# Kernel tuning notes

Measured on AMD Instinct MI355X. Metric: run time of the kernel, lower is better.

The kernel has to match this reference:

```python
import jax, jax.numpy as jnp
import numpy as np

N, C, H, W = 64, 64, 8, 8        # batch, img_net_out_dim, feature-map spatial dims
E = 256                           # ques_rnn_hidden_dim
G = 256                           # rn_g_dim
F_DIM = 256                       # rn_f_dim
NUM_CLASSES = 2
D = C + 2                         # per-object feature dim (channels + 2 loc coords)
G_IN = 2 * D + E                  # 388


def setup_inputs() -> dict:
    key = jax.random.key(0)
    ks = jax.random.split(key, 10)

    def w(k, shape):
        fan_in = shape[0]
        return jax.random.normal(k, shape, dtype=jnp.float32) / np.sqrt(fan_in).astype(np.float32)

    return {
        "img": jax.random.normal(ks[0], (N, C, H, W), dtype=jnp.float32),
        "ques": jax.random.normal(ks[1], (N, E), dtype=jnp.float32),
        "g_w1": w(ks[2], (G_IN, G)), "g_b1": jnp.zeros((G,), jnp.float32),
        "g_w2": w(ks[3], (G, G)),    "g_b2": jnp.zeros((G,), jnp.float32),
        "g_w3": w(ks[4], (G, G)),    "g_b3": jnp.zeros((G,), jnp.float32),
        "g_w4": w(ks[5], (G, G)),    "g_b4": jnp.zeros((G,), jnp.float32),
        "f_w1": w(ks[6], (G, F_DIM)),       "f_b1": jnp.zeros((F_DIM,), jnp.float32),
        "f_w2": w(ks[7], (F_DIM, F_DIM)),   "f_b2": jnp.zeros((F_DIM,), jnp.float32),
        "f_w3": w(ks[8], (F_DIM, NUM_CLASSES)), "f_b3": jnp.zeros((NUM_CLASSES,), jnp.float32),
    }


def _img_to_pairs(img, ques):
    # img: (N, C, H, W); ques: (N, E) -> pairs: (N, O*O, 2*(C+2)+E)
    n, c, h, w = img.shape
    o = h * w
    cells = img.reshape(n, c, o)
    idx = jnp.arange(o)
    loc = jnp.stack([idx // w, idx % w], axis=0).astype(img.dtype)      # (2, O)
    cells = jnp.concatenate([cells, jnp.broadcast_to(loc, (n, 2, o))], axis=1)  # (N, D, O)
    cells = cells.transpose(0, 2, 1)                                    # (N, O, D)
    d = cells.shape[-1]
    one = jnp.broadcast_to(cells[:, :, None, :], (n, o, o, d))          # object i
    two = jnp.broadcast_to(cells[:, None, :, :], (n, o, o, d))          # object j
    three = jnp.broadcast_to(ques[:, None, None, :], (n, o, o, ques.shape[-1]))
    pairs = jnp.concatenate([one, two, three], axis=-1)                 # (N, O, O, G_IN)
    return pairs.reshape(n, o * o, -1)


def reference(img, ques, g_w1, g_b1, g_w2, g_b2, g_w3, g_b3, g_w4, g_b4,
              f_w1, f_b1, f_w2, f_b2, f_w3, f_b3):
    n = img.shape[0]
    pairs = _img_to_pairs(img, ques)                  # (N, P, G_IN)
    x = pairs.reshape(-1, pairs.shape[-1])            # (N*P, G_IN)
    x = jax.nn.relu(x @ g_w1 + g_b1)
    x = jax.nn.relu(x @ g_w2 + g_b2)
    x = jax.nn.relu(x @ g_w3 + g_b3)
    x = jax.nn.relu(x @ g_w4 + g_b4)
    context = x.reshape(n, -1, x.shape[-1]).mean(axis=1)   # (N, G)
    # f MLP: Linear+ReLU, Linear+ReLU, Dropout(eval=identity), Linear
    y = jax.nn.relu(context @ f_w1 + f_b1)
    y = jax.nn.relu(y @ f_w2 + f_b2)
    scores = y @ f_w3 + f_b3                          # (N, 2)
    return jax.nn.log_softmax(scores, axis=1)
```

## Files before the change

kernel.cpp:

```cpp
#include <hip/hip_runtime.h>
#include <hip/hip_bf16.h>

typedef __bf16 bf16x8 __attribute__((ext_vector_type(8)));
typedef __bf16 bf16x4 __attribute__((ext_vector_type(4)));
typedef float  f32x4  __attribute__((ext_vector_type(4)));

__global__ __launch_bounds__(256) void prep_kernel(
    const float* __restrict__ img, const float* __restrict__ ques,
    const float* __restrict__ g_w1, const float* __restrict__ g_b1,
    const float* __restrict__ g_w2, const float* __restrict__ g_w3,
    const float* __restrict__ g_w4,
    float* __restrict__ U, float* __restrict__ V, float* __restrict__ Qb,
    __bf16* __restrict__ W2t, __bf16* __restrict__ W3t, __bf16* __restrict__ W4t) {
  __shared__ float smem[64 * 65];
  const int blk = blockIdx.x;
  const int t = threadIdx.x;

  if (blk < 256) {
    const int n = blk >> 2, obase = (blk & 3) * 16;
    for (int idx = t; idx < 66 * 16; idx += 256) {
      const int c = idx >> 4, o = obase + (idx & 15);
      float v;
      if (c < 64)      v = img[n * 4096 + c * 64 + o];
      else if (c == 64) v = (float)(o >> 3);
      else              v = (float)(o & 7);
      smem[idx] = v;
    }
    __syncthreads();
    float u[16], vv[16];
#pragma unroll
    for (int o = 0; o < 16; ++o) { u[o] = 0.f; vv[o] = 0.f; }
    for (int d = 0; d < 66; ++d) {
      const float wu = g_w1[d * 256 + t];
      const float wv = g_w1[(66 + d) * 256 + t];
#pragma unroll
      for (int o = 0; o < 16; ++o) {
        const float cc = smem[d * 16 + o];
        u[o]  += cc * wu;
        vv[o] += cc * wv;
      }
    }
#pragma unroll
    for (int o = 0; o < 16; ++o) {
      U[(size_t)(n * 64 + obase + o) * 256 + t] = u[o];
      V[(size_t)(n * 64 + obase + o) * 256 + t] = vv[o];
    }
  } else if (blk < 320) {
    const int n = blk - 256;
    smem[t] = ques[n * 256 + t];
    __syncthreads();
    float s = g_b1[t];
    for (int e = 0; e < 256; ++e) s += smem[e] * g_w1[(132 + e) * 256 + t];
    Qb[n * 256 + t] = s;
  } else {
    const int b2 = blk - 320;
    const int wsel = b2 >> 4;
    const int tile = b2 & 15;
    const int r0 = (tile >> 2) * 64, c0 = (tile & 3) * 64;
    const float* W = (wsel == 0) ? g_w2 : (wsel == 1) ? g_w3 : g_w4;
    __bf16* Wt    = (wsel == 0) ? W2t  : (wsel == 1) ? W3t  : W4t;
    const int col = t & 63, rb = (t >> 6) * 16;
#pragma unroll 4
    for (int j = 0; j < 16; ++j)
      smem[(rb + j) * 65 + col] = W[(size_t)(r0 + rb + j) * 256 + c0 + col];
    __syncthreads();
#pragma unroll 4
    for (int j = 0; j < 16; ++j)
      Wt[(size_t)(c0 + rb + j) * 256 + r0 + col] = (__bf16)smem[col * 65 + rb + j];
  }
}

__device__ __forceinline__ int hidx128(int row, int c) {
  const int kb = c >> 3;
  return kb * 1024 + (((row + kb) & 127) << 3) + (c & 7);
}

template <bool LAST>
__device__ __forceinline__ void g_layer(__bf16* Hs,
                                        bf16x8 ring[4][2],
                                        const __bf16* __restrict__ wcur,
                                        const __bf16* __restrict__ wnext,
                                        const float* __restrict__ bias_g,
                                        int nq, int q, int r16,
                                        float* __restrict__ pr0,
                                        float* __restrict__ pr1) {
  f32x4 acc[8][2];
  const f32x4 z = {0.f, 0.f, 0.f, 0.f};
#pragma unroll
  for (int m = 0; m < 8; ++m) {
    acc[m][0] = z;
    acc[m][1] = z;
  }

#pragma unroll
  for (int ks = 0; ks < 8; ++ks) {
    const int kb = ks * 4 + q;
    const bf16x8 b0 = ring[ks & 3][0];
    const bf16x8 b1 = ring[ks & 3][1];
    if (ks < 4) {
      ring[ks & 3][0] = *(const bf16x8*)(wcur + (ks + 4) * 32);
      ring[ks & 3][1] = *(const bf16x8*)(wcur + 4096 + (ks + 4) * 32);
    } else if (!LAST) {
      ring[ks & 3][0] = *(const bf16x8*)(wnext + (ks - 4) * 32);
      ring[ks & 3][1] = *(const bf16x8*)(wnext + 4096 + (ks - 4) * 32);
    }
#pragma unroll
    for (int m = 0; m < 8; ++m) {
      const int row = m * 16 + r16;
      const bf16x8 a = *(const bf16x8*)(&Hs[kb * 1024 + (((row + kb) & 127) << 3)]);
      acc[m][0] = __builtin_amdgcn_mfma_f32_16x16x32_bf16(b0, a, acc[m][0], 0, 0, 0);
      acc[m][1] = __builtin_amdgcn_mfma_f32_16x16x32_bf16(b1, a, acc[m][1], 0, 0, 0);
    }
  }

  f32x4 bv[2];
#pragma unroll
  for (int nt = 0; nt < 2; ++nt)
    bv[nt] = *(const f32x4*)&bias_g[nq * 32 + nt * 16 + q * 4];

  if (!LAST) {
    __syncthreads();
#pragma unroll
    for (int m = 0; m < 8; ++m)
#pragma unroll
      for (int nt = 0; nt < 2; ++nt) {
        const int cb = nq * 32 + nt * 16 + q * 4;
        const f32x4 s = acc[m][nt] + bv[nt];
        bf16x4 h;
#pragma unroll
        for (int r = 0; r < 4; ++r) h[r] = (__bf16)fmaxf(s[r], 0.f);
        *(bf16x4*)(&Hs[hidx128(m * 16 + r16, cb)]) = h;
      }
    __syncthreads();
  } else {
#pragma unroll
    for (int h = 0; h < 2; ++h) {
#pragma unroll
      for (int nt = 0; nt < 2; ++nt) {
        const int cb = nq * 32 + nt * 16 + q * 4;
        f32x4 s;
#pragma unroll
        for (int r = 0; r < 4; ++r)
          s[r] = fmaxf(acc[h * 4 + 0][nt][r] + bv[nt][r], 0.f)
               + fmaxf(acc[h * 4 + 1][nt][r] + bv[nt][r], 0.f)
               + fmaxf(acc[h * 4 + 2][nt][r] + bv[nt][r], 0.f)
               + fmaxf(acc[h * 4 + 3][nt][r] + bv[nt][r], 0.f);
#pragma unroll
        for (int d = 1; d < 16; d <<= 1) {
#pragma unroll
          for (int r = 0; r < 4; ++r) s[r] += __shfl_xor(s[r], d, 64);
        }
        if (r16 == 0) *(f32x4*)&(h ? pr1 : pr0)[cb] = s;
      }
    }
  }
}

__global__ __launch_bounds__(512, 3) void rn_main(
    const float* __restrict__ U, const float* __restrict__ V,
    const float* __restrict__ Qb,
    const __bf16* __restrict__ W2t, const __bf16* __restrict__ W3t,
    const __bf16* __restrict__ W4t,
    const float* __restrict__ b2, const float* __restrict__ b3,
    const float* __restrict__ b4,
    float* __restrict__ part) {
  __shared__ __align__(16) __bf16 Hs[32768];
  const int blk = blockIdx.x;
  const int nimg = blk >> 5, ipair = blk & 31;
  const int iobj0 = ipair * 2;
  const int t = threadIdx.x;
  const int nq = t >> 6, lane = t & 63;
  const int q = lane >> 4, r16 = lane & 15;

  const size_t woff = (size_t)(nq * 32 + r16) * 256 + q * 8;
  const __bf16* w2 = W2t + woff;
  const __bf16* w3 = W3t + woff;
  const __bf16* w4 = W4t + woff;

  bf16x8 ring[4][2];
#pragma unroll
  for (int d = 0; d < 4; ++d) {
    ring[d][0] = *(const bf16x8*)(w2 + d * 32);
    ring[d][1] = *(const bf16x8*)(w2 + 4096 + d * 32);
  }

  {
    const int c4 = t & 63;
    const int rb = t >> 6;
    const int isel = rb >> 2;
    const f32x4 u4 = *(const f32x4*)&U[(size_t)(nimg * 64 + iobj0 + isel) * 256 + c4 * 4];
    const f32x4 q4 = *(const f32x4*)&Qb[(size_t)nimg * 256 + c4 * 4];
    const f32x4 uq = u4 + q4;
#pragma unroll
    for (int jj = 0; jj < 16; ++jj) {
      const int row = rb * 16 + jj;
      const int j = (rb & 3) * 16 + jj;
      const f32x4 v4 = *(const f32x4*)&V[(size_t)(nimg * 64 + j) * 256 + c4 * 4];
      bf16x4 h;
#pragma unroll
      for (int r = 0; r < 4; ++r) h[r] = (__bf16)fmaxf(uq[r] + v4[r], 0.f);
      *(bf16x4*)(&Hs[hidx128(row, c4 * 4)]) = h;
    }
  }
  __syncthreads();

  float* pr0 = part + (size_t)blk * 512;
  float* pr1 = pr0 + 256;

  g_layer<false>(Hs, ring, w2, w3, b2, nq, q, r16, pr0, pr1);
  g_layer<false>(Hs, ring, w3, w4, b3, nq, q, r16, pr0, pr1);
  g_layer<true >(Hs, ring, w4, w4, b4, nq, q, r16, pr0, pr1);
}

__global__ __launch_bounds__(256) void rn_final(
    const float* __restrict__ part,
    const float* __restrict__ f_w1, const float* __restrict__ f_b1,
    const float* __restrict__ f_w2, const float* __restrict__ f_b2,
    const float* __restrict__ f_w3, const float* __restrict__ f_b3,
    float* __restrict__ out) {
  __shared__ float ctx[256], y1[256], y2[256], sc[2];
  const int n = blockIdx.x, t = threadIdx.x;

  float s = 0.f;
  for (int i = 0; i < 64; ++i) s += part[((size_t)n * 64 + i) * 256 + t];
  ctx[t] = s * (1.0f / 4096.0f);
  __syncthreads();

  float a = f_b1[t];
  for (int k = 0; k < 256; ++k) a += ctx[k] * f_w1[k * 256 + t];
  y1[t] = fmaxf(a, 0.f);
  __syncthreads();

  float b = f_b2[t];
  for (int k = 0; k < 256; ++k) b += y1[k] * f_w2[k * 256 + t];
  y2[t] = fmaxf(b, 0.f);
  __syncthreads();

  if (t < 2) {
    float c = f_b3[t];
    for (int k = 0; k < 256; ++k) c += y2[k] * f_w3[k * 2 + t];
    sc[t] = c;
  }
  __syncthreads();

  if (t == 0) {
    const float s0 = sc[0], s1 = sc[1];
    const float mx = fmaxf(s0, s1);
    const float lse = mx + logf(expf(s0 - mx) + expf(s1 - mx));
    out[n * 2 + 0] = s0 - lse;
    out[n * 2 + 1] = s1 - lse;
  }
}

extern "C" void kernel_launch(void* const* d_in, const int* in_sizes, int n_in,
                              void* d_out, int out_size, void* d_ws, size_t ws_size,
                              hipStream_t stream) {
  const float* img  = (const float*)d_in[0];
  const float* ques = (const float*)d_in[1];
  const float* g_w1 = (const float*)d_in[2];
  const float* g_b1 = (const float*)d_in[3];
  const float* g_w2 = (const float*)d_in[4];
  const float* g_b2 = (const float*)d_in[5];
  const float* g_w3 = (const float*)d_in[6];
  const float* g_b3 = (const float*)d_in[7];
  const float* g_w4 = (const float*)d_in[8];
  const float* g_b4 = (const float*)d_in[9];
  const float* f_w1 = (const float*)d_in[10];
  const float* f_b1 = (const float*)d_in[11];
  const float* f_w2 = (const float*)d_in[12];
  const float* f_b2 = (const float*)d_in[13];
  const float* f_w3 = (const float*)d_in[14];
  const float* f_b3 = (const float*)d_in[15];
  float* out = (float*)d_out;

  char* ws = (char*)d_ws;
  float*  U    = (float*)(ws);
  float*  V    = (float*)(ws + (size_t)4  * 1048576);
  float*  part = (float*)(ws + (size_t)8  * 1048576);
  float*  Qb   = (float*)(ws + (size_t)12 * 1048576);
  __bf16* W2t  = (__bf16*)(ws + (size_t)12 * 1048576 + 65536);
  __bf16* W3t  = W2t + 65536;
  __bf16* W4t  = W3t + 65536;

  prep_kernel<<<368, 256, 0, stream>>>(img, ques, g_w1, g_b1, g_w2, g_w3, g_w4,
                                       U, V, Qb, W2t, W3t, W4t);
  rn_main<<<2048, 512, 0, stream>>>(U, V, Qb, W2t, W3t, W4t, g_b2, g_b3, g_b4, part);
  rn_final<<<64, 256, 0, stream>>>(part, f_w1, f_b1, f_w2, f_b2, f_w3, f_b3, out);
}
```

Before: 255.7 us.

## Make rn_main persistent over 8 units with ping-pong LDS buffers

rn_main now launches 256 blocks, and each block loops over 8 (image, object-pair) units instead of launching one block per unit. LDS is doubled to two 64KB buffers that alternate between layers, which removes the barrier before each epilogue write. The last layer's epilogue overlaps building the next unit's input and prefetching the W2 ring. The doubled LDS (128KB per block) limits residency to one block per CU, and 256 blocks leave little slack for tail balance across CUs.

```diff
diff --git a/kernel.cpp b/kernel.cpp
--- a/kernel.cpp
+++ b/kernel.cpp
@@ -75,8 +75,32 @@
   return kb * 1024 + (((row + kb) & 127) << 3) + (c & 7);
 }
 
+__device__ __forceinline__ void phase0(const float* __restrict__ U,
+                                       const float* __restrict__ V,
+                                       const float* __restrict__ Qb,
+                                       int nimg, int iobj0, int t,
+                                       __bf16* __restrict__ buf) {
+  const int c4 = t & 63;
+  const int rb = t >> 6;
+  const int isel = rb >> 2;
+  const f32x4 u4 = *(const f32x4*)&U[(size_t)(nimg * 64 + iobj0 + isel) * 256 + c4 * 4];
+  const f32x4 q4 = *(const f32x4*)&Qb[(size_t)nimg * 256 + c4 * 4];
+  const f32x4 uq = u4 + q4;
+#pragma unroll
+  for (int jj = 0; jj < 16; ++jj) {
+    const int row = rb * 16 + jj;
+    const int j = (rb & 3) * 16 + jj;
+    const f32x4 v4 = *(const f32x4*)&V[(size_t)(nimg * 64 + j) * 256 + c4 * 4];
+    bf16x4 h;
+#pragma unroll
+    for (int r = 0; r < 4; ++r) h[r] = (__bf16)fmaxf(uq[r] + v4[r], 0.f);
+    *(bf16x4*)(&buf[hidx128(row, c4 * 4)]) = h;
+  }
+}
+
 template <bool LAST>
-__device__ __forceinline__ void g_layer(__bf16* Hs,
+__device__ __forceinline__ void g_layer(const __bf16* __restrict__ Rb,
+                                        __bf16* __restrict__ Wb,
                                         bf16x8 ring[4][2],
                                         const __bf16* __restrict__ wcur,
                                         const __bf16* __restrict__ wnext,
@@ -100,14 +124,14 @@
     if (ks < 4) {
       ring[ks & 3][0] = *(const bf16x8*)(wcur + (ks + 4) * 32);
       ring[ks & 3][1] = *(const bf16x8*)(wcur + 4096 + (ks + 4) * 32);
-    } else if (!LAST) {
+    } else {
       ring[ks & 3][0] = *(const bf16x8*)(wnext + (ks - 4) * 32);
       ring[ks & 3][1] = *(const bf16x8*)(wnext + 4096 + (ks - 4) * 32);
     }
 #pragma unroll
     for (int m = 0; m < 8; ++m) {
       const int row = m * 16 + r16;
-      const bf16x8 a = *(const bf16x8*)(&Hs[kb * 1024 + (((row + kb) & 127) << 3)]);
+      const bf16x8 a = *(const bf16x8*)(&Rb[kb * 1024 + (((row + kb) & 127) << 3)]);
       acc[m][0] = __builtin_amdgcn_mfma_f32_16x16x32_bf16(b0, a, acc[m][0], 0, 0, 0);
       acc[m][1] = __builtin_amdgcn_mfma_f32_16x16x32_bf16(b1, a, acc[m][1], 0, 0, 0);
     }
@@ -119,7 +143,6 @@
     bv[nt] = *(const f32x4*)&bias_g[nq * 32 + nt * 16 + q * 4];
 
   if (!LAST) {
-    __syncthreads();
 #pragma unroll
     for (int m = 0; m < 8; ++m)
 #pragma unroll
@@ -129,7 +152,7 @@
         bf16x4 h;
 #pragma unroll
         for (int r = 0; r < 4; ++r) h[r] = (__bf16)fmaxf(s[r], 0.f);
-        *(bf16x4*)(&Hs[hidx128(m * 16 + r16, cb)]) = h;
+        *(bf16x4*)(&Wb[hidx128(m * 16 + r16, cb)]) = h;
       }
     __syncthreads();
   } else {
@@ -164,10 +187,8 @@
     const float* __restrict__ b2, const float* __restrict__ b3,
     const float* __restrict__ b4,
     float* __restrict__ part) {
-  __shared__ __align__(16) __bf16 Hs[32768];
-  const int blk = blockIdx.x;
-  const int nimg = blk >> 5, ipair = blk & 31;
-  const int iobj0 = ipair * 2;
+  __shared__ __align__(16) __bf16 Hs[2 * 32768];
+  const int pblk = blockIdx.x;
   const int t = threadIdx.x;
   const int nq = t >> 6, lane = t & 63;
   const int q = lane >> 4, r16 = lane & 15;
@@ -184,32 +205,29 @@
     ring[d][1] = *(const bf16x8*)(w2 + 4096 + d * 32);
   }
 
-  {
-    const int c4 = t & 63;
-    const int rb = t >> 6;
-    const int isel = rb >> 2;
-    const f32x4 u4 = *(const f32x4*)&U[(size_t)(nimg * 64 + iobj0 + isel) * 256 + c4 * 4];
-    const f32x4 q4 = *(const f32x4*)&Qb[(size_t)nimg * 256 + c4 * 4];
-    const f32x4 uq = u4 + q4;
-#pragma unroll
-    for (int jj = 0; jj < 16; ++jj) {
-      const int row = rb * 16 + jj;
-      const int j = (rb & 3) * 16 + jj;
-      const f32x4 v4 = *(const f32x4*)&V[(size_t)(nimg * 64 + j) * 256 + c4 * 4];
-      bf16x4 h;
-#pragma unroll
-      for (int r = 0; r < 4; ++r) h[r] = (__bf16)fmaxf(uq[r] + v4[r], 0.f);
-      *(bf16x4*)(&Hs[hidx128(row, c4 * 4)]) = h;
-    }
-  }
-  __syncthreads();
-
-  float* pr0 = part + (size_t)blk * 512;
-  float* pr1 = pr0 + 256;
-
-  g_layer<false>(Hs, ring, w2, w3, b2, nq, q, r16, pr0, pr1);
-  g_layer<false>(Hs, ring, w3, w4, b3, nq, q, r16, pr0, pr1);
-  g_layer<true >(Hs, ring, w4, w4, b4, nq, q, r16, pr0, pr1);
+  const int unit0 = pblk * 8;
+
+  __bf16* A = Hs;
+  __bf16* B = Hs + 32768;
+
+  phase0(U, V, Qb, unit0 >> 5, (unit0 & 31) * 2, t, A);
+  __syncthreads();
+
+  for (int u = 0; u < 8; ++u) {
+    const int unit = unit0 + u;
+    float* pr0 = part + (size_t)unit * 512;
+    float* pr1 = pr0 + 256;
+
+    g_layer<false>(A, B, ring, w2, w3, b2, nq, q, r16, pr0, pr1);
+    g_layer<false>(B, A, ring, w3, w4, b3, nq, q, r16, pr0, pr1);
+    g_layer<true >(A, B, ring, w4, w2, b4, nq, q, r16, pr0, pr1);
+    if (u < 7) {
+      const int nu = unit + 1;
+      phase0(U, V, Qb, nu >> 5, (nu & 31) * 2, t, B);
+    }
+    __syncthreads();
+    __bf16* tmp = A; A = B; B = tmp;
+  }
 }
 
 __global__ __launch_bounds__(256) void rn_final(
@@ -284,6 +302,6 @@
 
   prep_kernel<<<368, 256, 0, stream>>>(img, ques, g_w1, g_b1, g_w2, g_w3, g_w4,
                                        U, V, Qb, W2t, W3t, W4t);
-  rn_main<<<2048, 512, 0, stream>>>(U, V, Qb, W2t, W3t, W4t, g_b2, g_b3, g_b4, part);
+  rn_main<<<256, 512, 0, stream>>>(U, V, Qb, W2t, W3t, W4t, g_b2, g_b3, g_b4, part);
   rn_final<<<64, 256, 0, stream>>>(part, f_w1, f_b1, f_w2, f_b2, f_w3, f_b3, out);
 }
```

After: 365.3 us. +42.9%, slower.
